# Kernel tuning notes

Hardware: AMD Instinct MI355X
Metric: run time of the kernel (lower is better)

Reference implementation:

```python
import jax, jax.numpy as jnp
import numpy as np

DE = 4   # encoder depth (de); ne+1 == de so all cells are used
DD = 4   # decoder depth (dd)
BS = 64
SL = 256
FL = 256
SI = 512
SH = 512  # must equal SI (original module requires it)


def setup_inputs() -> dict:
    key = jax.random.key(0)
    ks = jax.random.split(key, 8)
    s = 0.05  # init scale to keep gates out of saturation
    z4 = (DE, BS, SH)
    inp = {
        "x": jax.random.normal(ks[0], (BS, SL, SI), jnp.float32),
        "fl": FL,
        # gate order along last dim: [f, i, g, o], each of width SH
        "enc_W": jax.random.normal(ks[1], (DE, DE, SH, 4 * SH), jnp.float32) * s,
        "enc_V": jax.random.normal(ks[2], (DE, DE, SH, 4 * SH), jnp.float32) * s,
        "enc_b": jnp.zeros((DE, DE, 4 * SH), jnp.float32),
        "enc_h0": jnp.zeros(z4, jnp.float32),
        "enc_c0": jnp.zeros(z4, jnp.float32),
        "dec_W": jax.random.normal(ks[3], (DD, DD, SH, 4 * SH), jnp.float32) * s,
        "dec_V": jax.random.normal(ks[4], (DD, DD, SH, 4 * SH), jnp.float32) * s,
        "dec_b": jnp.zeros((DD, DD, 4 * SH), jnp.float32),
        "dec_h0": jnp.zeros((DD, BS, SH), jnp.float32),
        "dec_c0": jnp.zeros((DD, BS, SH), jnp.float32),
        "fin_W": jax.random.normal(ks[5], (SH, SI), jnp.float32) * s,
        "fin_b": jnp.zeros((SI,), jnp.float32),
    }
    return inp


def _lstm_cell(W, V, b, x, h, c):
    # fused gate GEMM: z = x@U + h@Vh + b, gates [f,i,g,o]
    z = x @ W + h @ V + b                      # (bs, 4*sh)
    f, i, g, o = jnp.split(z, 4, axis=-1)
    f = jax.nn.sigmoid(f)
    i = jax.nn.sigmoid(i)
    g = jnp.tanh(g)
    o = jax.nn.sigmoid(o)
    C = f * c + i * g
    H = o * jnp.tanh(C)
    return H, C


def _forward(x, fl, enc_W, enc_V, enc_b, enc_h0, enc_c0,
             dec_W, dec_V, dec_b, dec_h0, dec_c0, fin_W, fin_b):
    de = enc_W.shape[0]
    dd = dec_W.shape[0]

    def enc_step(carry, x_t):
        h, c = carry                            # (de, bs, sh) each
        for L in range(de):                     # over the de ModuleLists
            for e in range(de):                 # cells 0..de-1 within a list
                inp = x_t if e == 0 else h[e - 1]
                H, C = _lstm_cell(enc_W[L, e], enc_V[L, e], enc_b[L, e], inp, h[e], c[e])
                h = h.at[e].set(H)
                c = c.at[e].set(C)
        return (h, c), None

    (h_enc, _), _ = jax.lax.scan(enc_step, (enc_h0, enc_c0), jnp.swapaxes(x, 0, 1))
    state0 = h_enc[de - 1]                      # last updated encoder hidden

    def dec_step(carry, _):
        h, c, state = carry
        outs = []
        for L in range(dd):
            for e in range(dd):
                inp = state if e == 0 else h[e - 1]
                H, C = _lstm_cell(dec_W[L, e], dec_V[L, e], dec_b[L, e], inp, h[e], c[e])
                h = h.at[e].set(H)
                c = c.at[e].set(C)
            state = h[dd - 1]
            outs.append(state)                  # output appended per list, per step
        return (h, c, state), jnp.stack(outs)   # (dd, bs, sh)

    _, ys = jax.lax.scan(dec_step, (dec_h0, dec_c0, state0), None, length=fl)
    # ys: (fl, dd, bs, sh) -> (fl*dd, bs, sh) -> (bs, fl*dd, sh)
    out = ys.reshape(fl * dd, ys.shape[2], ys.shape[3]).transpose(1, 0, 2)
    return jax.nn.sigmoid(out @ fin_W + fin_b)  # (bs, fl*dd, si)


def reference(x, fl, enc_W, enc_V, enc_b, enc_h0, enc_c0,
              dec_W, dec_V, dec_b, dec_h0, dec_c0, fin_W, fin_b):
    return _forward(x, fl, enc_W, enc_V, enc_b, enc_h0, enc_c0,
                    dec_W, dec_V, dec_b, dec_h0, dec_c0, fin_W, fin_b)
```

## Files before the change

kernel.cpp:

```cpp
#include <hip/hip_runtime.h>

typedef _Float16 f16;
typedef _Float16 f16x8 __attribute__((ext_vector_type(8)));
typedef float f32x4 __attribute__((ext_vector_type(4)));

#define BS 64
#define SL 256
#define FL 256
#define SI 512
#define SH 512
#define NBLK 256
#define ESTEPS 1027

__device__ __forceinline__ float sigmoidf_(float x) { return 1.f / (1.f + __expf(-x)); }
__device__ __forceinline__ float tanhf_(float x) { float e = __expf(2.f * x); return 1.f - 2.f / (e + 1.f); }

__device__ __forceinline__ f16x8 ldg_cohere(const f16* p) {
  f16x8 r;
  asm volatile("global_load_dwordx4 %0, %1, off sc0 sc1"
               : "=v"(r) : "v"(p) : "memory");
  return r;
}

__global__ void conv_w(const float* __restrict__ W, const float* __restrict__ V,
                       f16* __restrict__ out) {
  long idx = (long)blockIdx.x * blockDim.x + threadIdx.x;
  int j    = (int)(idx & 7);
  int lane = (int)((idx >> 3) & 63);
  int kk   = (int)((idx >> 9) & 15);
  int kh   = (int)((idx >> 13) & 1);
  int g    = (int)((idx >> 14) & 3);
  int nt   = (int)((idx >> 16) & 31);
  long cell = idx >> 21;
  int n = g * 512 + nt * 16 + (lane & 15);
  int k = kh * 512 + kk * 32 + (lane >> 4) * 8 + j;
  float v = (k < 512) ? W[(cell * 512 + k) * 2048 + n]
                      : V[(cell * 512 + (k - 512)) * 2048 + n];
  out[idx] = (f16)v;
}

__global__ void conv_x(const float* __restrict__ x, f16* __restrict__ xt) {
  long idx = (long)blockIdx.x * blockDim.x + threadIdx.x;
  int i = (int)(idx & 511);
  int b = (int)((idx >> 9) & 63);
  int t = (int)(idx >> 15);
  xt[idx] = (f16)x[((long)b * SL + t) * SI + i];
}

__global__ void conv_fin(const float* __restrict__ finW, f16* __restrict__ fint) {
  long idx = (long)blockIdx.x * blockDim.x + threadIdx.x;
  int k = (int)(idx & 511);
  int n = (int)(idx >> 9);
  fint[idx] = (f16)finW[(long)k * SI + n];
}

__global__ void init_state(const float* __restrict__ h0e, const float* __restrict__ h0d,
                           f16* __restrict__ h_enc, f16* __restrict__ h_dec) {
  long idx = (long)blockIdx.x * blockDim.x + threadIdx.x;
  f16 he = (f16)h0e[idx];
  h_enc[idx] = he;
  h_enc[idx + 131072] = he;
  h_dec[idx + 131072] = (f16)h0d[idx];
}

__device__ __forceinline__ void store_h_agent(f16* p, float v) {
  f16 h = (f16)v;
  __hip_atomic_store((unsigned short*)p, __builtin_bit_cast(unsigned short, h),
                     __ATOMIC_RELAXED, __HIP_MEMORY_SCOPE_AGENT);
}

#define VMCNT0() do {                                                             \
    asm volatile("s_waitcnt vmcnt(0)" ::: "memory");                              \
    __builtin_amdgcn_sched_barrier(0);                                            \
  } while (0)

#define RAWBAR() do {                                                             \
    asm volatile("s_waitcnt lgkmcnt(0)" ::: "memory");                            \
    __builtin_amdgcn_sched_barrier(0);                                            \
    __builtin_amdgcn_s_barrier();                                                 \
    __builtin_amdgcn_sched_barrier(0);                                            \
  } while (0)

#define WAVE_ORDER() do {                                                          \
    asm volatile("s_waitcnt vmcnt(16)" ::: "memory");                              \
    __builtin_amdgcn_sched_barrier(0);                                             \
  } while (0)

#define END_STEP(TARGET) do {                                                      \
    __builtin_amdgcn_s_barrier();                                                  \
    asm volatile("" ::: "memory");                                                 \
    if (tid == 0)                                                                  \
      __hip_atomic_store(&bar[bflag], (TARGET), __ATOMIC_RELAXED,                  \
                         __HIP_MEMORY_SCOPE_AGENT);                                \
    if (wid == 0) {                                                                \
      for (;;) {                                                                   \
        int a0 = __hip_atomic_load(&bar[pf0], __ATOMIC_RELAXED,                    \
                                   __HIP_MEMORY_SCOPE_AGENT);                      \
        int a1 = __hip_atomic_load(&bar[pf1], __ATOMIC_RELAXED,                    \
                                   __HIP_MEMORY_SCOPE_AGENT);                      \
        int a2 = __hip_atomic_load(&bar[pf2], __ATOMIC_RELAXED,                    \
                                   __HIP_MEMORY_SCOPE_AGENT);                      \
        int a3 = __hip_atomic_load(&bar[pf3], __ATOMIC_RELAXED,                    \
                                   __HIP_MEMORY_SCOPE_AGENT);                      \
        if (a0 >= (TARGET) && a1 >= (TARGET) && a2 >= (TARGET) && a3 >= (TARGET))  \
          break;                                                                   \
        __builtin_amdgcn_s_sleep(2);                                               \
      }                                                                            \
    }                                                                              \
    __builtin_amdgcn_s_barrier();                                                  \
    asm volatile("" ::: "memory");                                                 \
    __builtin_amdgcn_sched_barrier(0);                                             \
  } while (0)

#define ENC_BODY(DD, P, TARGET) do {                                               \
    const int v = (DD) - eslot;                                                    \
    if (v >= 0 && v < 1024) {                                                      \
      const int L = v & 3, t = v >> 2;                                             \
      const f16* inp = (eslot == 0) ? (xt + (long)t * HSz)                         \
                                    : (h_enc + ((P)*4 + (eslot - 1)) * HSz);       \
      const f16* hin = h_enc + ((P)*4 + eslot) * HSz;                              \
      f16* hout = h_enc + ((1 - (P))*4 + eslot) * HSz;                             \
      {               \
        const f16* sA = inp + emt * 16384 + tid * 32;                              \
        f16x8 t0 = ldg_cohere(sA + 0),  t1 = ldg_cohere(sA + 8);                   \
        f16x8 t2 = ldg_cohere(sA + 16), t3 = ldg_cohere(sA + 24);                  \
        VMCNT0();                                                                  \
        f16* d = &As[0][tid >> 4][(tid & 15) * 32];                                \
        *(f16x8*)(d) = t0; *(f16x8*)(d + 8) = t1;                                  \
        *(f16x8*)(d + 16) = t2; *(f16x8*)(d + 24) = t3;                            \
        const f16* sB = hin + emt * 16384 + tid * 32;                              \
        t0 = ldg_cohere(sB + 0);  t1 = ldg_cohere(sB + 8);                         \
        t2 = ldg_cohere(sB + 16); t3 = ldg_cohere(sB + 24);                        \
        VMCNT0();                                                                  \
        f16* d2 = &As[1][tid >> 4][(tid & 15) * 32];                               \
        *(f16x8*)(d2) = t0; *(f16x8*)(d2 + 8) = t1;                                \
        *(f16x8*)(d2 + 16) = t2; *(f16x8*)(d2 + 24) = t3;                          \
      }                                                                            \
      RAWBAR();                                                                    \
      f32x4 acc0 = 0.f, acc1 = 0.f;                                                \
      _Pragma("unroll")                                                            \
      for (int kk = 0; kk < 16; ++kk) {                                            \
        f16x8 a0 = *(const f16x8*)&As[kh][col][kk * 32 + kg * 8];                  \
        f16x8 a1 = *(const f16x8*)&As[kh][16 + col][kk * 32 + kg * 8];             \
        acc0 = __builtin_amdgcn_mfma_f32_16x16x32_f16(a0, B[kk], acc0, 0,0,0);     \
        acc1 = __builtin_amdgcn_mfma_f32_16x16x32_f16(a1, B[kk], acc1, 0,0,0);     \
      }                                                                            \
      RAWBAR();        \
      _Pragma("unroll")                                                            \
      for (int r = 0; r < 4; ++r) {                                                \
        zred[wid][kg*4 + r][col] = acc0[r];                                        \
        zred[wid][16 + kg*4 + r][col] = acc1[r];                                   \
      }                                                                            \
      RAWBAR();                                                                    \
      {                                                                            \
        const int row = tid >> 4, ci = tid & 15, n = n0 + ci;                      \
        const float* bl = bias_enc_lds + L * 64 + ci;                              \
        float zf = bl[0]  + zred[0][row][ci] + zred[4][row][ci];                   \
        float zi = bl[16] + zred[1][row][ci] + zred[5][row][ci];                   \
        float zg = bl[32] + zred[2][row][ci] + zred[6][row][ci];                   \
        float zo = bl[48] + zred[3][row][ci] + zred[7][row][ci];                   \
        float f_ = sigmoidf_(zf), i_ = sigmoidf_(zi);                              \
        float g_ = tanhf_(zg),   o_ = sigmoidf_(zo);                               \
        const int grow = emt * 32 + row;                                           \
        float cin = (v == 0) ? enc_c0[(long)eslot * HSz + grow * SH + n] : ce;     \
        float cc = f_ * cin + i_ * g_;                                             \
        ce = cc;                                                                   \
        store_h_agent(hout + grow * SH + n, o_ * tanhf_(cc));                      \
      }                                                                            \
      const f16* wn = (v + 1 < 1024)                                               \
          ? wt_enc + ((long)(((v + 1) & 3) * 4 + eslot) << 21) + wslice            \
          : wt_dec + wslice;                                                       \
      asm volatile("" ::: "memory");                                               \
      _Pragma("unroll")                                                            \
      for (int kk = 0; kk < 16; ++kk) B[kk] = *(const f16x8*)(wn + kk * 512);      \
      WAVE_ORDER();                                                                \
    }                                                                              \
    END_STEP(TARGET);                                                              \
  } while (0)

#define DEC_BODY(E, CD, TARGET) do {                                               \
    const f16* inp;                                                                \
    if ((E) == 0)                                                                  \
      inp = (vv == 0) ? state0 : h_dec + ((par ^ 1) * 4 + 3) * HSz;                \
    else                                                                           \
      inp = h_dec + (par * 4 + (E) - 1) * HSz;                                     \
    const f16* hin = h_dec + ((par ^ 1) * 4 + (E)) * HSz;                          \
    f16* hout = h_dec + (par * 4 + (E)) * HSz;                                     \
    {                                                                              \
      const int idx16 = tid * 16;                                                  \
      const int ch = idx16 >> 12;                                                  \
      const int off = idx16 & 4095;                                                \
      const f16* src = (ch ? hin : inp) + dmt * 4096 + off;                        \
      f16x8 t0 = ldg_cohere(src), t1 = ldg_cohere(src + 8);                        \
      VMCNT0();                                                                    \
      f16* d = &As[ch][off >> 9][off & 511];                                       \
      *(f16x8*)(d) = t0; *(f16x8*)(d + 8) = t1;                                    \
    }                                                                              \
    RAWBAR();                                                                      \
    f32x4 acc = 0.f;                                                               \
    _Pragma("unroll")                                                              \
    for (int kk = 0; kk < 16; ++kk) {                                              \
      f16x8 a = *(const f16x8*)&As[kh][col & 7][kk * 32 + kg * 8];                 \
      acc = __builtin_amdgcn_mfma_f32_16x16x32_f16(a, B[kk], acc, 0,0,0);          \
    }                                                                              \
    RAWBAR();              \
    if (kg < 2) {                                                                  \
      _Pragma("unroll")                                                            \
      for (int r = 0; r < 4; ++r) zred[wid][kg*4 + r][col] = acc[r];               \
    }                                                                              \
    RAWBAR();                                                                      \
    if (tid < 128) {                                                               \
      const int row = tid >> 4, ci = tid & 15, n = n0 + ci;                        \
      const float* bl = bias_dec_lds + (L * 4 + (E)) * 64 + ci;                    \
      float zf = bl[0]  + zred[0][row][ci] + zred[4][row][ci];                     \
      float zi = bl[16] + zred[1][row][ci] + zred[5][row][ci];                     \
      float zg = bl[32] + zred[2][row][ci] + zred[6][row][ci];                     \
      float zo = bl[48] + zred[3][row][ci] + zred[7][row][ci];                     \
      float f_ = sigmoidf_(zf), i_ = sigmoidf_(zi);                                \
      float g_ = tanhf_(zg),   o_ = sigmoidf_(zo);                                 \
      const int grow = dmt * 8 + row;                                              \
      float cin = (vv == 0) ? dec_c0[(long)(E) * HSz + grow * SH + n] : CD;        \
      float cc = f_ * cin + i_ * g_;                                               \
      CD = cc;                                                                     \
      float hv = o_ * tanhf_(cc);                                                  \
      store_h_agent(hout + grow * SH + n, hv);                                     \
      if ((E) == 3) ys[((long)grow * 1024 + vv) * SH + n] = (f16)hv;               \
    }                                                                              \
    {                                                                              \
      const int Lp = ((E) < 3) ? L : ((vv + 1) & 3);                               \
      const int Ep = ((E) + 1) & 3;                                                \
      const f16* wn = wt_dec + ((long)(Lp * 4 + Ep) << 21) + wslice;               \
      asm volatile("" ::: "memory");                                               \
      _Pragma("unroll")                                                            \
      for (int kk = 0; kk < 16; ++kk) B[kk] = *(const f16x8*)(wn + kk * 512);      \
      WAVE_ORDER();                                                                \
    }                                                                              \
    END_STEP(TARGET);                                                              \
  } while (0)

__global__ __launch_bounds__(512, 2) void lstm_persist(
    const f16* __restrict__ xt,
    const f16* __restrict__ wt_enc, const f16* __restrict__ wt_dec,
    const float* __restrict__ enc_b, const float* __restrict__ dec_b,
    const float* __restrict__ enc_c0, const float* __restrict__ dec_c0,
    f16* __restrict__ h_enc, f16* __restrict__ h_dec,
    f16* __restrict__ ys, int* __restrict__ bar) {
  const int tid = threadIdx.x;
  const int lane = tid & 63;
  const int wid = tid >> 6;
  const int g = wid & 3;
  const int kh = wid >> 2;
  const int col = lane & 15;
  const int kg = lane >> 4;
  const int idx = blockIdx.x;
  const int nt = idx & 31;
  const int n0 = nt << 4;
  const int eslot = idx >> 6;
  const int emt = (idx >> 5) & 1;
  const int dmt = idx >> 5;

  const int bflag = idx * 32;
  const int pf0 = (lane * 4 + 0) * 32;
  const int pf1 = (lane * 4 + 1) * 32;
  const int pf2 = (lane * 4 + 2) * 32;
  const int pf3 = (lane * 4 + 3) * 32;

  __shared__ __align__(16) char ubuf[2 * 32 * 520 * 2];
  f16 (*const As)[32][520] = (f16(*)[32][520])ubuf;
  float (*const zred)[32][17] = (float(*)[32][17])ubuf;
  __shared__ float bias_enc_lds[4 * 4 * 16];
  __shared__ float bias_dec_lds[16 * 4 * 16];

  const long wslice = ((long)(nt * 4 + g) * 2 + kh) * 8192 + lane * 8;
  const int HSz = BS * SH;
  const f16* const state0 = h_enc + (1 * 4 + 3) * HSz;

  for (int i = tid; i < 256; i += 512) {
    int L = i >> 6, gg = (i >> 4) & 3, ci = i & 15;
    bias_enc_lds[i] = enc_b[(L * 4 + eslot) * 2048 + gg * 512 + n0 + ci];
  }
  for (int i = tid; i < 1024; i += 512) {
    int cell = i >> 6, gg = (i >> 4) & 3, ci = i & 15;
    bias_dec_lds[i] = dec_b[cell * 2048 + gg * 512 + n0 + ci];
  }

  f16x8 B[16];
  {
    const f16* w = wt_enc + ((long)eslot << 21) + wslice;
#pragma unroll
    for (int kk = 0; kk < 16; ++kk) B[kk] = *(const f16x8*)(w + kk * 512);
  }
  __syncthreads();

  float ce = 0.f;
  float cd0 = 0.f, cd1 = 0.f, cd2 = 0.f, cd3 = 0.f;

  for (int d = 0;; d += 2) {
    ENC_BODY(d, 0, d + 1);
    if (d == 1026) break;
    ENC_BODY(d + 1, 1, d + 2);
  }

  for (int vv = 0; vv < 1024; ++vv) {
    const int L = vv & 3, par = vv & 1;
    DEC_BODY(0, cd0, ESTEPS + vv * 4 + 1);
    DEC_BODY(1, cd1, ESTEPS + vv * 4 + 2);
    DEC_BODY(2, cd2, ESTEPS + vv * 4 + 3);
    DEC_BODY(3, cd3, ESTEPS + vv * 4 + 4);
  }
}

__global__ __launch_bounds__(256) void final_gemm(const f16* __restrict__ ys,
                                                  const f16* __restrict__ fint,
                                                  const float* __restrict__ finb,
                                                  float* __restrict__ out) {
  const int lane = threadIdx.x & 63;
  const int w = threadIdx.x >> 6;
  const int col = lane & 15;
  const int kg = lane >> 4;
  const long m0 = (long)blockIdx.y * 64;
  const int n0 = (blockIdx.x * 4 + w) * 16;

  f32x4 acc[4];
#pragma unroll
  for (int mi = 0; mi < 4; ++mi) acc[mi] = 0.f;

#pragma unroll 2
  for (int kk = 0; kk < 16; ++kk) {
    f16x8 b = *(const f16x8*)(fint + (long)(n0 + col) * 512 + kk * 32 + kg * 8);
#pragma unroll
    for (int mi = 0; mi < 4; ++mi) {
      f16x8 a = *(const f16x8*)(ys + (m0 + mi * 16 + col) * 512 + kk * 32 + kg * 8);
      acc[mi] = __builtin_amdgcn_mfma_f32_16x16x32_f16(a, b, acc[mi], 0, 0, 0);
    }
  }
  const int n = n0 + col;
  const float bn = finb[n];
#pragma unroll
  for (int mi = 0; mi < 4; ++mi)
#pragma unroll
    for (int r = 0; r < 4; ++r)
      out[(m0 + mi * 16 + kg * 4 + r) * 512 + n] = sigmoidf_(acc[mi][r] + bn);
}

extern "C" void kernel_launch(void* const* d_in, const int* in_sizes, int n_in,
                              void* d_out, int out_size, void* d_ws, size_t ws_size,
                              hipStream_t stream) {
  const float* x      = (const float*)d_in[0];
  const float* enc_W  = (const float*)d_in[2];
  const float* enc_V  = (const float*)d_in[3];
  const float* enc_b  = (const float*)d_in[4];
  const float* enc_h0 = (const float*)d_in[5];
  const float* enc_c0 = (const float*)d_in[6];
  const float* dec_W  = (const float*)d_in[7];
  const float* dec_V  = (const float*)d_in[8];
  const float* dec_b  = (const float*)d_in[9];
  const float* dec_h0 = (const float*)d_in[10];
  const float* dec_c0 = (const float*)d_in[11];
  const float* fin_W  = (const float*)d_in[12];
  const float* fin_b  = (const float*)d_in[13];
  float* out = (float*)d_out;

  f16* wt_enc = (f16*)d_ws;
  f16* wt_dec = wt_enc + (long)16 * 2048 * 1024;
  f16* xt     = wt_dec + (long)16 * 2048 * 1024;
  f16* fint   = xt + (long)SL * BS * SI;
  f16* ys     = fint + (long)SH * SI;
  f16* h_enc  = ys + (long)BS * (FL * 4) * SH;
  f16* h_dec  = h_enc + (long)2 * 4 * BS * SH;
  float* c_unused = (float*)(h_dec + (long)2 * 4 * BS * SH);
  int* bar = (int*)(c_unused + (long)8 * BS * SH);

  hipMemsetAsync(bar, 0, 65536, stream);

  conv_w<<<131072, 256, 0, stream>>>(enc_W, enc_V, wt_enc);
  conv_w<<<131072, 256, 0, stream>>>(dec_W, dec_V, wt_dec);
  conv_x<<<32768, 256, 0, stream>>>(x, xt);
  conv_fin<<<1024, 256, 0, stream>>>(fin_W, fint);
  init_state<<<512, 256, 0, stream>>>(enc_h0, dec_h0, h_enc, h_dec);

  lstm_persist<<<NBLK, 512, 0, stream>>>(xt, wt_enc, wt_dec, enc_b, dec_b,
                                         enc_c0, dec_c0, h_enc, h_dec, ys, bar);

  dim3 fg(8, 1024);
  final_gemm<<<fg, 256, 0, stream>>>(ys, fint, fin_b, out);
}
```

Measured before the change: 24.71 ms.

## Narrow grid barriers to true dependencies and swizzle LDS staging buffers

Replaces the all-blocks spin barrier with dependency-scoped waits: encoder blocks wait only on the flags of the 64 blocks that produce their row half, and decoder blocks only on the 32 blocks sharing their row tile. One full barrier is kept at the encoder/decoder boundary. The A-tile LDS layout becomes XOR-swizzled instead of padded, and zred gets its own buffer, which removes the second block barrier per step. This cuts per-step global sync latency and LDS bank conflicts, at the cost of more LDS and subtle correctness risk from the narrower dependency sets.

```diff
diff --git a/kernel.cpp b/kernel.cpp
--- a/kernel.cpp
+++ b/kernel.cpp
@@ -10,7 +10,7 @@
 #define SI 512
 #define SH 512
 #define NBLK 256
-#define ESTEPS 1027
+#define TFULL 1028
 
 __device__ __forceinline__ float sigmoidf_(float x) { return 1.f / (1.f + __expf(-x)); }
 __device__ __forceinline__ float tanhf_(float x) { float e = __expf(2.f * x); return 1.f - 2.f / (e + 1.f); }
@@ -69,6 +69,8 @@
                      __ATOMIC_RELAXED, __HIP_MEMORY_SCOPE_AGENT);
 }
 
+#define SWZ(ROW, BOFF) (((ROW) << 10) + ((BOFF) ^ ((((ROW) & 7)) << 4)))
+
 #define VMCNT0() do {                                                             \
     asm volatile("s_waitcnt vmcnt(0)" ::: "memory");                              \
     __builtin_amdgcn_sched_barrier(0);                                            \
@@ -86,7 +88,44 @@
     __builtin_amdgcn_sched_barrier(0);                                             \
   } while (0)
 
-#define END_STEP(TARGET) do {                                                      \
+#define END_STEP_ENC(TARGET) do {                                                  \
+    __builtin_amdgcn_s_barrier();                                                  \
+    asm volatile("" ::: "memory");                                                 \
+    if (tid == 0)                                                                  \
+      __hip_atomic_store(&bar[bflag], (TARGET), __ATOMIC_RELAXED,                  \
+                         __HIP_MEMORY_SCOPE_AGENT);                                \
+    if (wid == 0) {                                                                \
+      for (;;) {                                                                   \
+        int a0 = __hip_atomic_load(&bar[pe0], __ATOMIC_RELAXED,                    \
+                                   __HIP_MEMORY_SCOPE_AGENT);                      \
+        int a1 = __hip_atomic_load(&bar[pe1], __ATOMIC_RELAXED,                    \
+                                   __HIP_MEMORY_SCOPE_AGENT);                      \
+        if (a0 >= (TARGET) && a1 >= (TARGET)) break;                               \
+        __builtin_amdgcn_s_sleep(1);                                               \
+      }                                                                            \
+    }                                                                              \
+    __builtin_amdgcn_s_barrier();                                                  \
+    asm volatile("" ::: "memory");                                                 \
+    __builtin_amdgcn_sched_barrier(0);                                             \
+  } while (0)
+
+#define END_STEP_DEC(TARGET) do {                                                  \
+    __builtin_amdgcn_s_barrier();                                                  \
+    asm volatile("" ::: "memory");                                                 \
+    if (tid == 0)                                                                  \
+      __hip_atomic_store(&bar[bflag], (TARGET), __ATOMIC_RELAXED,                  \
+                         __HIP_MEMORY_SCOPE_AGENT);                                \
+    if (wid == 0) {                                                                \
+      while (__hip_atomic_load(&bar[pd], __ATOMIC_RELAXED,                         \
+                               __HIP_MEMORY_SCOPE_AGENT) < (TARGET))               \
+        __builtin_amdgcn_s_sleep(1);                                               \
+    }                                                                              \
+    __builtin_amdgcn_s_barrier();                                                  \
+    asm volatile("" ::: "memory");                                                 \
+    __builtin_amdgcn_sched_barrier(0);                                             \
+  } while (0)
+
+#define END_STEP_FULL(TARGET) do {                                                 \
     __builtin_amdgcn_s_barrier();                                                  \
     asm volatile("" ::: "memory");                                                 \
     if (tid == 0)                                                                  \
@@ -120,32 +159,35 @@
                                     : (h_enc + ((P)*4 + (eslot - 1)) * HSz);       \
       const f16* hin = h_enc + ((P)*4 + eslot) * HSz;                              \
       f16* hout = h_enc + ((1 - (P))*4 + eslot) * HSz;                             \
-      {               \
-        const f16* sA = inp + emt * 16384 + tid * 32;                              \
-        f16x8 t0 = ldg_cohere(sA + 0),  t1 = ldg_cohere(sA + 8);                   \
-        f16x8 t2 = ldg_cohere(sA + 16), t3 = ldg_cohere(sA + 24);                  \
+      {        \
+        const f16* c0p = inp + emt * 16384;                                        \
+        const f16* c1p = hin + emt * 16384;                                        \
+        f16x8 tr[8];                                                               \
+        _Pragma("unroll")                                                          \
+        for (int k2 = 0; k2 < 4; ++k2) {                                           \
+          const int s = tid + k2 * 512, row = s >> 6, c16 = s & 63;                \
+          tr[k2]     = ldg_cohere(c0p + row * 512 + c16 * 8);                      \
+          tr[k2 + 4] = ldg_cohere(c1p + row * 512 + c16 * 8);                      \
+        }                                                                          \
         VMCNT0();                                                                  \
-        f16* d = &As[0][tid >> 4][(tid & 15) * 32];                                \
-        *(f16x8*)(d) = t0; *(f16x8*)(d + 8) = t1;                                  \
-        *(f16x8*)(d + 16) = t2; *(f16x8*)(d + 24) = t3;                            \
-        const f16* sB = hin + emt * 16384 + tid * 32;                              \
-        t0 = ldg_cohere(sB + 0);  t1 = ldg_cohere(sB + 8);                         \
-        t2 = ldg_cohere(sB + 16); t3 = ldg_cohere(sB + 24);                        \
-        VMCNT0();                                                                  \
-        f16* d2 = &As[1][tid >> 4][(tid & 15) * 32];                               \
-        *(f16x8*)(d2) = t0; *(f16x8*)(d2 + 8) = t1;                                \
-        *(f16x8*)(d2 + 16) = t2; *(f16x8*)(d2 + 24) = t3;                          \
+        _Pragma("unroll")                                                          \
+        for (int k2 = 0; k2 < 4; ++k2) {                                           \
+          const int s = tid + k2 * 512, row = s >> 6, c16 = s & 63;                \
+          *(f16x8*)(AsBuf + SWZ(row, c16 * 16)) = tr[k2];                          \
+          *(f16x8*)(AsBuf + 32768 + SWZ(row, c16 * 16)) = tr[k2 + 4];              \
+        }                                                                          \
       }                                                                            \
       RAWBAR();                                                                    \
       f32x4 acc0 = 0.f, acc1 = 0.f;                                                \
       _Pragma("unroll")                                                            \
       for (int kk = 0; kk < 16; ++kk) {                                            \
-        f16x8 a0 = *(const f16x8*)&As[kh][col][kk * 32 + kg * 8];                  \
-        f16x8 a1 = *(const f16x8*)&As[kh][16 + col][kk * 32 + kg * 8];             \
+        f16x8 a0 = *(const f16x8*)(AsBuf + kh * 32768 +                            \
+                                   SWZ(col, kk * 64 + kg * 16));                   \
+        f16x8 a1 = *(const f16x8*)(AsBuf + kh * 32768 +                            \
+                                   SWZ(col + 16, kk * 64 + kg * 16));              \
         acc0 = __builtin_amdgcn_mfma_f32_16x16x32_f16(a0, B[kk], acc0, 0,0,0);     \
         acc1 = __builtin_amdgcn_mfma_f32_16x16x32_f16(a1, B[kk], acc1, 0,0,0);     \
       }                                                                            \
-      RAWBAR();        \
       _Pragma("unroll")                                                            \
       for (int r = 0; r < 4; ++r) {                                                \
         zred[wid][kg*4 + r][col] = acc0[r];                                        \
@@ -175,7 +217,7 @@
       for (int kk = 0; kk < 16; ++kk) B[kk] = *(const f16x8*)(wn + kk * 512);      \
       WAVE_ORDER();                                                                \
     }                                                                              \
-    END_STEP(TARGET);                                                              \
+    END_STEP_ENC(TARGET);                                                          \
   } while (0)
 
 #define DEC_BODY(E, CD, TARGET) do {                                               \
@@ -187,23 +229,21 @@
     const f16* hin = h_dec + ((par ^ 1) * 4 + (E)) * HSz;                          \
     f16* hout = h_dec + (par * 4 + (E)) * HSz;                                     \
     {                                                                              \
-      const int idx16 = tid * 16;                                                  \
-      const int ch = idx16 >> 12;                                                  \
-      const int off = idx16 & 4095;                                                \
-      const f16* src = (ch ? hin : inp) + dmt * 4096 + off;                        \
-      f16x8 t0 = ldg_cohere(src), t1 = ldg_cohere(src + 8);                        \
+      const int drow = tid >> 6, dc16 = tid & 63;                                  \
+      f16x8 t0 = ldg_cohere(inp + dmt * 4096 + drow * 512 + dc16 * 8);             \
+      f16x8 t1 = ldg_cohere(hin + dmt * 4096 + drow * 512 + dc16 * 8);             \
       VMCNT0();                                                                    \
-      f16* d = &As[ch][off >> 9][off & 511];                                       \
-      *(f16x8*)(d) = t0; *(f16x8*)(d + 8) = t1;                                    \
+      *(f16x8*)(AsBuf + SWZ(drow, dc16 * 16)) = t0;                                \
+      *(f16x8*)(AsBuf + 8192 + SWZ(drow, dc16 * 16)) = t1;                         \
     }                                                                              \
     RAWBAR();                                                                      \
     f32x4 acc = 0.f;                                                               \
     _Pragma("unroll")                                                              \
     for (int kk = 0; kk < 16; ++kk) {                                              \
-      f16x8 a = *(const f16x8*)&As[kh][col & 7][kk * 32 + kg * 8];                 \
+      f16x8 a = *(const f16x8*)(AsBuf + kh * 8192 +                                \
+                                SWZ(col & 7, kk * 64 + kg * 16));                  \
       acc = __builtin_amdgcn_mfma_f32_16x16x32_f16(a, B[kk], acc, 0,0,0);          \
     }                                                                              \
-    RAWBAR();              \
     if (kg < 2) {                                                                  \
       _Pragma("unroll")                                                            \
       for (int r = 0; r < 4; ++r) zred[wid][kg*4 + r][col] = acc[r];               \
@@ -235,7 +275,7 @@
       for (int kk = 0; kk < 16; ++kk) B[kk] = *(const f16x8*)(wn + kk * 512);      \
       WAVE_ORDER();                                                                \
     }                                                                              \
-    END_STEP(TARGET);                                                              \
+    END_STEP_DEC(TARGET);                                                          \
   } while (0)
 
 __global__ __launch_bounds__(512, 2) void lstm_persist(
@@ -260,14 +300,16 @@
   const int dmt = idx >> 5;
 
   const int bflag = idx * 32;
+  const int pe0 = ((((lane) >> 5) << 6) | (emt << 5) | (lane & 31)) * 32;
+  const int pe1 = (((((lane + 64)) >> 5) << 6) | (emt << 5) | ((lane + 64) & 31)) * 32;
+  const int pd = (dmt * 32 + (lane & 31)) * 32;
   const int pf0 = (lane * 4 + 0) * 32;
   const int pf1 = (lane * 4 + 1) * 32;
   const int pf2 = (lane * 4 + 2) * 32;
   const int pf3 = (lane * 4 + 3) * 32;
 
-  __shared__ __align__(16) char ubuf[2 * 32 * 520 * 2];
-  f16 (*const As)[32][520] = (f16(*)[32][520])ubuf;
-  float (*const zred)[32][17] = (float(*)[32][17])ubuf;
+  __shared__ __align__(16) char AsBuf[65536];
+  __shared__ float zred[8][32][17];
   __shared__ float bias_enc_lds[4 * 4 * 16];
   __shared__ float bias_dec_lds[16 * 4 * 16];
 
@@ -301,12 +343,14 @@
     ENC_BODY(d + 1, 1, d + 2);
   }
 
+  END_STEP_FULL(TFULL);
+
   for (int vv = 0; vv < 1024; ++vv) {
     const int L = vv & 3, par = vv & 1;
-    DEC_BODY(0, cd0, ESTEPS + vv * 4 + 1);
-    DEC_BODY(1, cd1, ESTEPS + vv * 4 + 2);
-    DEC_BODY(2, cd2, ESTEPS + vv * 4 + 3);
-    DEC_BODY(3, cd3, ESTEPS + vv * 4 + 4);
+    DEC_BODY(0, cd0, TFULL + vv * 4 + 1);
+    DEC_BODY(1, cd1, TFULL + vv * 4 + 2);
+    DEC_BODY(2, cd2, TFULL + vv * 4 + 3);
+    DEC_BODY(3, cd3, TFULL + vv * 4 + 4);
   }
 }
 
```

Result: faster. 20.50 ms (-17.0%).
